# Performance work log

Measured on AMD Instinct MI355X. Metric: run time of the kernel, lower is better.

## Reference

```python
import jax, jax.numpy as jnp
import numpy as np

W = 5      # window size
H = 4      # num heads (num_channels)
EPS = 1e-6

def rmsnorm(x, w):
    return x * w * jax.lax.rsqrt(jnp.mean(x * x, axis=-1, keepdims=True) + EPS)

def dwconv3d(x, k):
    # x: [B,D0,D1,D2,C], k: [3,3,3,1,C] depthwise 3x3x3 conv, SAME padding
    return jax.lax.conv_general_dilated(
        x, k, (1, 1, 1), 'SAME',
        dimension_numbers=('NDHWC', 'DHWIO', 'NDHWC'),
        feature_group_count=x.shape[-1])

def _part(t):
    # [B,D0,D1,D2,C] -> [B*nw, W^3, C] non-overlapping 3D windows
    B, D0, D1, D2, C = t.shape
    t = t.reshape(B, D0 // W, W, D1 // W, W, D2 // W, W, C)
    t = t.transpose(0, 1, 3, 5, 2, 4, 6, 7)
    return t.reshape(-1, W ** 3, C)

def _unpart(t, B, D0, D1, D2):
    C = t.shape[-1]
    t = t.reshape(B, D0 // W, D1 // W, D2 // W, W, W, W, C)
    t = t.transpose(0, 1, 4, 2, 5, 3, 6, 7)
    return t.reshape(B, D0, D1, D2, C)

def _pool01(t):
    # mean-pool poolable_dims=(0,1) by factor W -> coarse grid
    B, D0, D1, D2, C = t.shape
    return t.reshape(B, D0 // W, W, D1 // W, W, D2, C).mean(axis=(2, 4))

def _mha(q, k, v):
    # q,k,v: [N, L, C] -> [N, L, C] multi-head attention
    N, L, C = q.shape
    dh = C // H
    q = q.reshape(N, L, H, dh)
    k = k.reshape(N, L, H, dh)
    v = v.reshape(N, L, H, dh)
    s = jnp.einsum('nqhd,nkhd->nhqk', q, k) * (1.0 / np.sqrt(dh))
    p = jax.nn.softmax(s, axis=-1)
    return jnp.einsum('nhqk,nkhd->nqhd', p, v).reshape(N, L, C)

def _hier_attn(x, qkv_w, qkv_b, proj_w, proj_b, dw_pre, dw_post, lr_down, lr_up):
    B, D0, D1, D2, C = x.shape
    # conv_position='both': pre depthwise-conv positional term
    xin = x + dwconv3d(x, dw_pre)
    qkv = xin @ qkv_w + qkv_b                     # [B,D0,D1,D2,3C]
    q, k, v = jnp.split(qkv, 3, axis=-1)
    # fine scale: windowed local attention in W^3 blocks
    fine = _unpart(_mha(_part(q), _part(k), _part(v)), B, D0, D1, D2)
    # coarse scale: pool dims (0,1) by W, global attention over coarse tokens
    qc, kc, vc = _pool01(q), _pool01(k), _pool01(v)
    Nc = qc.shape[1] * qc.shape[2] * qc.shape[3]
    oc = _mha(qc.reshape(B, Nc, C), kc.reshape(B, Nc, C), vc.reshape(B, Nc, C))
    oc = oc.reshape(B, D0 // W, D1 // W, D2, C)
    oc = jnp.repeat(jnp.repeat(oc, W, axis=1), W, axis=2)   # upsample to full grid
    # lowrank hierarchical merge of coarse branch into fine branch
    merged = fine + (oc @ lr_down) @ lr_up
    out = merged @ proj_w + proj_b
    out = out + xin                               # attn_residual
    out = out + dwconv3d(out, dw_post)            # post conv position
    return out

def setup_inputs() -> dict:
    key = jax.random.key(0)
    ks = jax.random.split(key, 8)
    B, D0, D1, D2, C = 4, 40, 40, 20, 256
    rank = C // 4
    s = 0.02
    return {
        'x': jax.random.normal(ks[0], (B, D0, D1, D2, C), jnp.float32),
        'norm1_w': jnp.ones((C,), jnp.float32),
        'attn_norm_w': jnp.ones((C,), jnp.float32),
        'qkv_w': jax.random.normal(ks[1], (C, 3 * C), jnp.float32) * s,
        'qkv_b': jnp.zeros((3 * C,), jnp.float32),
        'proj_w': jax.random.normal(ks[2], (C, C), jnp.float32) * s,
        'proj_b': jnp.zeros((C,), jnp.float32),
        'dw_pre': jax.random.normal(ks[3], (3, 3, 3, 1, C), jnp.float32) * s,
        'dw_post': jax.random.normal(ks[4], (3, 3, 3, 1, C), jnp.float32) * s,
        'lr_down': jax.random.normal(ks[5], (C, rank), jnp.float32) * s,
        'lr_up': jax.random.normal(ks[6], (rank, C), jnp.float32) * s,
    }

def reference(x, norm1_w, attn_norm_w, qkv_w, qkv_b, proj_w, proj_b,
              dw_pre, dw_post, lr_down, lr_up) -> jnp.ndarray:
    # x = x + attn_norm(hier_attn(norm1(x)))   (dropout inactive in eval)
    a = _hier_attn(rmsnorm(x, norm1_w), qkv_w, qkv_b, proj_w, proj_b,
                   dw_pre, dw_post, lr_down, lr_up)
    return x + rmsnorm(a, attn_norm_w)
```

## Files before the change

### kernel.cpp

```cpp
#include <hip/hip_runtime.h>

#define D0c 40
#define D1c 40
#define D2c 20
#define NVOX 128000

typedef __attribute__((ext_vector_type(4))) float f4;
typedef __attribute__((ext_vector_type(8))) __bf16 bf8;
typedef __attribute__((ext_vector_type(8))) unsigned short u8s;

static __device__ __forceinline__ unsigned short f2bf(float f) {
  union { float f; unsigned int u; } v; v.f = f;
  unsigned int r = v.u + 0x7fffu + ((v.u >> 16) & 1u);
  return (unsigned short)(r >> 16);
}
static __device__ __forceinline__ float bf2f(unsigned short h) {
  union { unsigned int u; float f; } v; v.u = ((unsigned int)h) << 16;
  return v.f;
}

#define MFMA16(a, b, c) __builtin_amdgcn_mfma_f32_16x16x32_bf16((a), (b), (c), 0, 0, 0)

static __device__ __forceinline__ void gload16(const void* g, void* l) {
  __builtin_amdgcn_global_load_lds((const __attribute__((address_space(1))) unsigned int*)g,
                                   (__attribute__((address_space(3))) unsigned int*)l, 16, 0, 0);
}

__global__ __launch_bounds__(256) void k_prepw(const float* __restrict__ qkv_w,
                                               const float* __restrict__ proj_w,
                                               unsigned short* __restrict__ wq,
                                               unsigned short* __restrict__ wp) {
  int id = blockIdx.x * 256 + threadIdx.x;
  if (id < 768 * 256) {
    int kk = id & 31, row = (id >> 5) & 127, kc = (id >> 12) & 7, nt = id >> 15;
    int s = kk >> 3, kj = kk & 7;
    int g = s ^ ((row >> 1) & 3);
    int k = kc * 32 + g * 8 + kj;
    int n = nt * 128 + row;
    wq[id] = f2bf(qkv_w[k * 768 + n]);
  } else {
    int j = id - 768 * 256;
    int kk = j & 31, row = (j >> 5) & 127, kc = (j >> 12) & 7, nt = j >> 15;
    int s = kk >> 3, kj = kk & 7;
    int g = s ^ ((row >> 1) & 3);
    int k = kc * 32 + g * 8 + kj;
    int n = nt * 128 + row;
    wp[j] = f2bf(proj_w[k * 256 + n]);
  }
}

__global__ __launch_bounds__(256) void k_rms1(const float* __restrict__ x,
                                              const float* __restrict__ w,
                                              unsigned short* __restrict__ xn) {
  int wv = threadIdx.x >> 6, ln = threadIdx.x & 63;
  int n = blockIdx.x * 4 + wv;
  f4 v = ((const f4*)(x + (size_t)n * 256))[ln];
  float ss = v.x * v.x + v.y * v.y + v.z * v.z + v.w * v.w;
#pragma unroll
  for (int m = 32; m >= 1; m >>= 1) ss += __shfl_xor(ss, m);
  float rs = rsqrtf(ss * (1.f / 256.f) + 1e-6f);
  f4 wv4 = ((const f4*)w)[ln];
  ushort4 o;
  o.x = f2bf(v.x * wv4.x * rs); o.y = f2bf(v.y * wv4.y * rs);
  o.z = f2bf(v.z * wv4.z * rs); o.w = f2bf(v.w * wv4.w * rs);
  ((ushort4*)(xn + (size_t)n * 256))[ln] = o;
}

__global__ __launch_bounds__(256) void k_convpre(const unsigned short* __restrict__ xn,
                                                 const float* __restrict__ dw,
                                                 unsigned short* __restrict__ xin) {
  int ch = threadIdx.x;
  int col = blockIdx.x;
  int z1 = col % D1c; int t = col / D1c; int z0 = t % D0c; int b = t / D0c;

  float W[27];
#pragma unroll
  for (int k = 0; k < 27; k++) W[k] = dw[k * 256 + ch];

  const unsigned short* base[9];
  bool val[9];
#pragma unroll
  for (int c = 0; c < 9; c++) {
    int dy = c / 3 - 1, dx = c % 3 - 1;
    int y0 = z0 + dy, y1 = z1 + dx;
    val[c] = ((unsigned)y0 < (unsigned)D0c) && ((unsigned)y1 < (unsigned)D1c);
    int yy0 = val[c] ? y0 : z0, yy1 = val[c] ? y1 : z1;
    base[c] = xn + ((size_t)((b * D0c + yy0) * D1c + yy1) * D2c) * 256 + ch;
  }
  float a0 = 0.f, a1 = 0.f, a2 = 0.f;
  unsigned short nxt[9];
#pragma unroll
  for (int c = 0; c < 9; c++) nxt[c] = val[c] ? base[c][0] : (unsigned short)0;
  unsigned short* op = xin + ((size_t)col * D2c) * 256 + ch;

  for (int z = 0; z < 20; z++) {
    float cf[9];
#pragma unroll
    for (int c = 0; c < 9; c++) cf[c] = bf2f(nxt[c]);
    int zn = (z < 19) ? (z + 1) : 19;
#pragma unroll
    for (int c = 0; c < 9; c++)
      nxt[c] = val[c] ? base[c][(size_t)zn * 256] : (unsigned short)0;
#pragma unroll
    for (int c = 0; c < 9; c++) {
      a0 += W[c * 3 + 2] * cf[c];
      a1 += W[c * 3 + 1] * cf[c];
      a2 += W[c * 3 + 0] * cf[c];
    }
    a1 += cf[4];
    if (z >= 1) {
      *op = f2bf(a0);
      op += 256;
    }
    a0 = a1; a1 = a2; a2 = 0.f;
  }
  *op = f2bf(a0);
}

__global__ __launch_bounds__(256) void k_gemm_qkv(const unsigned short* __restrict__ a_bf,
                                                  const unsigned short* __restrict__ wq2,
                                                  const float* __restrict__ bias,
                                                  unsigned short* __restrict__ out) {
  __shared__ unsigned short As[16384];
  __shared__ unsigned short Bs[8192];
  int m0 = blockIdx.x * 64;
  int tid = threadIdx.x;
  int w = tid >> 6, l = tid & 63;
  int wr = w >> 1, wc = w & 1;
  int lrow = l & 15, lg = l >> 4;

  {
    const char* Ab = (const char*)(a_bf + (size_t)m0 * 256);
    int row = tid >> 2, s = tid & 3;
    int g = s ^ ((row >> 1) & 3);
    const char* src0 = Ab + row * 512 + g * 16;
    char* dst0 = ((char*)As) + w * 1024 + l * 16;
#pragma unroll
    for (int kc = 0; kc < 8; kc++)
      gload16(src0 + kc * 64, dst0 + kc * 4096);
  }
  {
    const char* gB = (const char*)wq2;
    char* lB = (char*)Bs;
    gload16(gB + tid * 16, lB + w * 1024 + l * 16);
    gload16(gB + 4096 + tid * 16, lB + 4096 + w * 1024 + l * 16);
  }

  int buf = 0;
  f4 acc[2][4];
  for (int nt = 0; nt < 6; nt++) {
    float bvv[4];
#pragma unroll
    for (int j = 0; j < 4; j++) bvv[j] = bias[nt * 128 + wc * 64 + j * 16 + lrow];
#pragma unroll
    for (int i = 0; i < 2; i++)
#pragma unroll
      for (int j = 0; j < 4; j++) acc[i][j] = {0.f, 0.f, 0.f, 0.f};

    for (int kc = 0; kc < 8; kc++) {
      int t = nt * 8 + kc;
      if (t + 1 < 48) {
        const char* gB = (const char*)wq2 + (size_t)(t + 1) * 8192;
        char* lB = ((char*)Bs) + (buf ^ 1) * 8192;
        gload16(gB + tid * 16, lB + w * 1024 + l * 16);
        gload16(gB + 4096 + tid * 16, lB + 4096 + w * 1024 + l * 16);
        asm volatile("s_waitcnt vmcnt(2)\n\ts_barrier" ::: "memory");
      } else {
        asm volatile("s_waitcnt vmcnt(0)\n\ts_barrier" ::: "memory");
      }
      bf8 af[2], bf_[4];
#pragma unroll
      for (int i = 0; i < 2; i++) {
        int row = wr * 32 + i * 16 + lrow;
        af[i] = *(const bf8*)&As[kc * 2048 + row * 32 + ((lg ^ ((row >> 1) & 3)) * 8)];
      }
#pragma unroll
      for (int j = 0; j < 4; j++) {
        int rowb = wc * 64 + j * 16 + lrow;
        bf_[j] = *(const bf8*)&Bs[buf * 4096 + rowb * 32 + ((lg ^ ((rowb >> 1) & 3)) * 8)];
      }
#pragma unroll
      for (int i = 0; i < 2; i++)
#pragma unroll
        for (int j = 0; j < 4; j++) acc[i][j] = MFMA16(af[i], bf_[j], acc[i][j]);
      asm volatile("s_barrier" ::: "memory");
      buf ^= 1;
    }

    unsigned short* Cs = &Bs[(buf ^ 1) * 4096];
    int crow = tid >> 3, cseg = tid & 7;
#pragma unroll
    for (int h = 0; h < 2; h++) {
      if (wr == h) {
#pragma unroll
        for (int i = 0; i < 2; i++)
#pragma unroll
          for (int j = 0; j < 4; j++)
#pragma unroll
            for (int r = 0; r < 4; r++)
              Cs[(i * 16 + lg * 4 + r) * 128 + wc * 64 + j * 16 + lrow] =
                  f2bf(acc[i][j][r] + bvv[j]);
      }
      asm volatile("s_waitcnt lgkmcnt(0)\n\ts_barrier" ::: "memory");
      {
        u8s v0 = *(const u8s*)&Cs[crow * 128 + cseg * 16];
        u8s v1 = *(const u8s*)&Cs[crow * 128 + cseg * 16 + 8];
        unsigned short* orow = out + (size_t)(m0 + h * 32 + crow) * 768 + nt * 128 + cseg * 16;
        *(u8s*)orow = v0;
        *(u8s*)(orow + 8) = v1;
      }
      asm volatile("s_waitcnt lgkmcnt(0)\n\ts_barrier" ::: "memory");
    }
  }
}

__global__ __launch_bounds__(256) void k_fineattn(const unsigned short* __restrict__ qkv,
                                                  unsigned short* __restrict__ fine) {
  __shared__ unsigned short sm[27136];
  unsigned short* Qs = sm;
  unsigned short* Ks = sm + 9216;
  unsigned short* Vt = sm + 18432;
  unsigned short* Ps = sm;
  int h = blockIdx.x & 3, wid = blockIdx.x >> 2;
  int w2 = wid & 3, w1 = (wid >> 2) & 7, w0 = (wid >> 5) & 7, b = wid >> 8;
  int tid = threadIdx.x;
  int tok = tid >> 1, half = tid & 1;
  if (tok < 125) {
    int i0 = tok / 25, rr = tok % 25, i1 = rr / 5, i2 = rr % 5;
    int n = ((b * D0c + w0 * 5 + i0) * D1c + w1 * 5 + i1) * D2c + w2 * 5 + i2;
    const u8s* qp = (const u8s*)(qkv + (size_t)n * 768 + h * 64 + half * 32);
    const u8s* kp = (const u8s*)(qkv + (size_t)n * 768 + 256 + h * 64 + half * 32);
    const unsigned short* vp = qkv + (size_t)n * 768 + 512 + h * 64 + half * 32;
#pragma unroll
    for (int e = 0; e < 4; e++) {
      *(u8s*)&Qs[tok * 72 + half * 32 + e * 8] = qp[e];
      *(u8s*)&Ks[tok * 72 + half * 32 + e * 8] = kp[e];
    }
#pragma unroll
    for (int d = 0; d < 32; d++) Vt[(half * 32 + d) * 136 + tok] = vp[d];
  } else {
    u8s z = {0, 0, 0, 0, 0, 0, 0, 0};
#pragma unroll
    for (int e = 0; e < 4; e++) {
      *(u8s*)&Qs[tok * 72 + half * 32 + e * 8] = z;
      *(u8s*)&Ks[tok * 72 + half * 32 + e * 8] = z;
    }
#pragma unroll
    for (int d = 0; d < 32; d++) Vt[(half * 32 + d) * 136 + tok] = 0;
  }
  __syncthreads();
  int wv = tid >> 6, ln = tid & 63, lrow = ln & 15, lg = ln >> 4;
  f4 s[2][8];
#pragma unroll
  for (int mi = 0; mi < 2; mi++)
#pragma unroll
    for (int ni = 0; ni < 8; ni++) s[mi][ni] = {0.f, 0.f, 0.f, 0.f};
  bf8 aq[2][2];
#pragma unroll
  for (int ks = 0; ks < 2; ks++)
#pragma unroll
    for (int mi = 0; mi < 2; mi++)
      aq[mi][ks] = *(const bf8*)&Qs[(wv * 32 + mi * 16 + lrow) * 72 + ks * 32 + lg * 8];
#pragma unroll
  for (int ni = 0; ni < 8; ni++) {
#pragma unroll
    for (int ks = 0; ks < 2; ks++) {
      bf8 bk = *(const bf8*)&Ks[(ni * 16 + lrow) * 72 + ks * 32 + lg * 8];
      s[0][ni] = MFMA16(aq[0][ks], bk, s[0][ni]);
      s[1][ni] = MFMA16(aq[1][ks], bk, s[1][ni]);
    }
  }
#pragma unroll
  for (int mi = 0; mi < 2; mi++) {
#pragma unroll
    for (int j = 0; j < 4; j++) {
      float mx = -3e38f;
#pragma unroll
      for (int ni = 0; ni < 8; ni++) {
        int col = ni * 16 + lrow;
        float v = (col < 125) ? s[mi][ni][j] * 0.125f : -3e38f;
        s[mi][ni][j] = v;
        mx = fmaxf(mx, v);
      }
#pragma unroll
      for (int m = 8; m >= 1; m >>= 1) mx = fmaxf(mx, __shfl_xor(mx, m));
      float sum = 0.f;
#pragma unroll
      for (int ni = 0; ni < 8; ni++) {
        float p = __expf(s[mi][ni][j] - mx);
        s[mi][ni][j] = p;
        sum += p;
      }
#pragma unroll
      for (int m = 8; m >= 1; m >>= 1) sum += __shfl_xor(sum, m);
      float inv = 1.f / sum;
#pragma unroll
      for (int ni = 0; ni < 8; ni++) s[mi][ni][j] *= inv;
    }
  }
  __syncthreads();
#pragma unroll
  for (int mi = 0; mi < 2; mi++)
#pragma unroll
    for (int ni = 0; ni < 8; ni++)
#pragma unroll
      for (int j = 0; j < 4; j++)
        Ps[(wv * 32 + mi * 16 + lg * 4 + j) * 136 + ni * 16 + lrow] = f2bf(s[mi][ni][j]);
  __syncthreads();
  f4 o[2][4];
#pragma unroll
  for (int mi = 0; mi < 2; mi++)
#pragma unroll
    for (int ni = 0; ni < 4; ni++) o[mi][ni] = {0.f, 0.f, 0.f, 0.f};
#pragma unroll
  for (int ks = 0; ks < 4; ks++) {
    bf8 ap0 = *(const bf8*)&Ps[(wv * 32 + 0 + lrow) * 136 + ks * 32 + lg * 8];
    bf8 ap1 = *(const bf8*)&Ps[(wv * 32 + 16 + lrow) * 136 + ks * 32 + lg * 8];
#pragma unroll
    for (int ni = 0; ni < 4; ni++) {
      bf8 bv = *(const bf8*)&Vt[(ni * 16 + lrow) * 136 + ks * 32 + lg * 8];
      o[0][ni] = MFMA16(ap0, bv, o[0][ni]);
      o[1][ni] = MFMA16(ap1, bv, o[1][ni]);
    }
  }
#pragma unroll
  for (int mi = 0; mi < 2; mi++) {
    int rt0 = wv * 32 + mi * 16 + lg * 4;
#pragma unroll
    for (int r = 0; r < 4; r++) {
      int tk = rt0 + r;
      if (tk >= 125) continue;
      int i0 = tk / 25, rr = tk % 25, i1 = rr / 5, i2 = rr % 5;
      int n = ((b * D0c + w0 * 5 + i0) * D1c + w1 * 5 + i1) * D2c + w2 * 5 + i2;
#pragma unroll
      for (int ni = 0; ni < 4; ni++)
        fine[(size_t)n * 256 + h * 64 + ni * 16 + lrow] = f2bf(o[mi][ni][r]);
    }
  }
}

__global__ __launch_bounds__(128) void k_pool(const unsigned short* __restrict__ qkv,
                                              unsigned short* __restrict__ qc,
                                              unsigned short* __restrict__ kc,
                                              unsigned short* __restrict__ vct) {
  int ct = blockIdx.x;
  int tid = threadIdx.x;
  if (tid >= 96) return;
  int z2 = ct % 20; int t = ct / 20; int c1 = t & 7; int c0 = (t >> 3) & 7; int b = t >> 6;
  int off = tid * 8;
  f4 s0 = {0.f, 0.f, 0.f, 0.f}, s1 = {0.f, 0.f, 0.f, 0.f};
  for (int i0 = 0; i0 < 5; i0++)
    for (int i1 = 0; i1 < 5; i1++) {
      int n = ((b * D0c + c0 * 5 + i0) * D1c + c1 * 5 + i1) * D2c + z2;
      u8s v = *(const u8s*)(qkv + (size_t)n * 768 + off);
      s0.x += bf2f(v[0]); s0.y += bf2f(v[1]); s0.z += bf2f(v[2]); s0.w += bf2f(v[3]);
      s1.x += bf2f(v[4]); s1.y += bf2f(v[5]); s1.z += bf2f(v[6]); s1.w += bf2f(v[7]);
    }
  const float sc = 1.f / 25.f;
  s0.x *= sc; s0.y *= sc; s0.z *= sc; s0.w *= sc;
  s1.x *= sc; s1.y *= sc; s1.z *= sc; s1.w *= sc;
  if (off < 512) {
    unsigned short* dst = (off < 256) ? (qc + (size_t)ct * 256 + off)
                                      : (kc + (size_t)ct * 256 + (off - 256));
    u8s o;
    o[0] = f2bf(s0.x); o[1] = f2bf(s0.y); o[2] = f2bf(s0.z); o[3] = f2bf(s0.w);
    o[4] = f2bf(s1.x); o[5] = f2bf(s1.y); o[6] = f2bf(s1.z); o[7] = f2bf(s1.w);
    *(u8s*)dst = o;
  } else {
    int vch = off - 512;
    int h = vch >> 6, d0 = vch & 63;
    int tk = ct - b * 1280;
    unsigned short* vb = vct + (((size_t)b * 4 + h) * 64 + d0) * 1288 + tk;
    vb[0 * 1288] = f2bf(s0.x); vb[1 * 1288] = f2bf(s0.y);
    vb[2 * 1288] = f2bf(s0.z); vb[3 * 1288] = f2bf(s0.w);
    vb[4 * 1288] = f2bf(s1.x); vb[5 * 1288] = f2bf(s1.y);
    vb[6 * 1288] = f2bf(s1.z); vb[7 * 1288] = f2bf(s1.w);
  }
}

__global__ __launch_bounds__(256) void k_coarse(const unsigned short* __restrict__ qc,
                                                const unsigned short* __restrict__ kc,
                                                const unsigned short* __restrict__ vct,
                                                float* __restrict__ oc) {
  __shared__ unsigned short Qs[9216];
  __shared__ unsigned short KP[9216];
  __shared__ unsigned short Vts[4608];
  int qt = blockIdx.x;
  int b = blockIdx.y >> 2, h = blockIdx.y & 3;
  int tid = threadIdx.x, wv = tid >> 6, ln = tid & 63, lrow = ln & 15, lg = ln >> 4;
  {
    int tk = tid >> 1, half = tid & 1;
    const u8s* qp = (const u8s*)(qc + (size_t)(b * 1280 + qt * 128 + tk) * 256 + h * 64 + half * 32);
#pragma unroll
    for (int e = 0; e < 4; e++) *(u8s*)&Qs[tk * 72 + half * 32 + e * 8] = qp[e];
  }
  float mrun[2][4], srun[2][4];
  f4 o[2][4];
#pragma unroll
  for (int mi = 0; mi < 2; mi++)
#pragma unroll
    for (int j = 0; j < 4; j++) { mrun[mi][j] = -3e38f; srun[mi][j] = 0.f; }
#pragma unroll
  for (int mi = 0; mi < 2; mi++)
#pragma unroll
    for (int ni = 0; ni < 4; ni++) o[mi][ni] = {0.f, 0.f, 0.f, 0.f};

  int ktok = tid >> 2, kq = (tid & 3) * 16;
  int vd = tid >> 2, vtc = (tid & 3) * 16;

  for (int kt = 0; kt < 20; kt++) {
    {
      const u8s* kp = (const u8s*)(kc + (size_t)(b * 1280 + kt * 64 + ktok) * 256 + h * 64 + kq);
      *(u8s*)&KP[ktok * 72 + kq] = kp[0];
      *(u8s*)&KP[ktok * 72 + kq + 8] = kp[1];
      const u8s* vp = (const u8s*)(vct + (((size_t)b * 4 + h) * 64 + vd) * 1288 + kt * 64 + vtc);
      *(u8s*)&Vts[vd * 72 + vtc] = vp[0];
      *(u8s*)&Vts[vd * 72 + vtc + 8] = vp[1];
    }
    __syncthreads();
    f4 s[2][4];
#pragma unroll
    for (int mi = 0; mi < 2; mi++)
#pragma unroll
      for (int ni = 0; ni < 4; ni++) s[mi][ni] = {0.f, 0.f, 0.f, 0.f};
    bf8 aq[2][2];
#pragma unroll
    for (int ks = 0; ks < 2; ks++)
#pragma unroll
      for (int mi = 0; mi < 2; mi++)
        aq[mi][ks] = *(const bf8*)&Qs[(wv * 32 + mi * 16 + lrow) * 72 + ks * 32 + lg * 8];
#pragma unroll
    for (int ni = 0; ni < 4; ni++) {
#pragma unroll
      for (int ks = 0; ks < 2; ks++) {
        bf8 bk = *(const bf8*)&KP[(ni * 16 + lrow) * 72 + ks * 32 + lg * 8];
        s[0][ni] = MFMA16(aq[0][ks], bk, s[0][ni]);
        s[1][ni] = MFMA16(aq[1][ks], bk, s[1][ni]);
      }
    }
#pragma unroll
    for (int mi = 0; mi < 2; mi++) {
#pragma unroll
      for (int j = 0; j < 4; j++) {
        float mx = -3e38f;
#pragma unroll
        for (int ni = 0; ni < 4; ni++) {
          float v = s[mi][ni][j] * 0.125f;
          s[mi][ni][j] = v;
          mx = fmaxf(mx, v);
        }
#pragma unroll
        for (int m = 8; m >= 1; m >>= 1) mx = fmaxf(mx, __shfl_xor(mx, m));
        float nm = fmaxf(mrun[mi][j], mx);
        float alpha = __expf(mrun[mi][j] - nm);
        mrun[mi][j] = nm;
        float sum = 0.f;
#pragma unroll
        for (int ni = 0; ni < 4; ni++) {
          float p = __expf(s[mi][ni][j] - nm);
          s[mi][ni][j] = p;
          sum += p;
        }
#pragma unroll
        for (int m = 8; m >= 1; m >>= 1) sum += __shfl_xor(sum, m);
        srun[mi][j] = srun[mi][j] * alpha + sum;
#pragma unroll
        for (int ni = 0; ni < 4; ni++) o[mi][ni][j] *= alpha;
      }
    }
    __syncthreads();
#pragma unroll
    for (int mi = 0; mi < 2; mi++)
#pragma unroll
      for (int ni = 0; ni < 4; ni++)
#pragma unroll
        for (int j = 0; j < 4; j++)
          KP[(wv * 32 + mi * 16 + lg * 4 + j) * 72 + ni * 16 + lrow] = f2bf(s[mi][ni][j]);
    __syncthreads();
#pragma unroll
    for (int ks = 0; ks < 2; ks++) {
      bf8 ap0 = *(const bf8*)&KP[(wv * 32 + 0 + lrow) * 72 + ks * 32 + lg * 8];
      bf8 ap1 = *(const bf8*)&KP[(wv * 32 + 16 + lrow) * 72 + ks * 32 + lg * 8];
#pragma unroll
      for (int ni = 0; ni < 4; ni++) {
        bf8 bv = *(const bf8*)&Vts[(ni * 16 + lrow) * 72 + ks * 32 + lg * 8];
        o[0][ni] = MFMA16(ap0, bv, o[0][ni]);
        o[1][ni] = MFMA16(ap1, bv, o[1][ni]);
      }
    }
    __syncthreads();
  }
#pragma unroll
  for (int mi = 0; mi < 2; mi++)
#pragma unroll
    for (int j = 0; j < 4; j++) {
      float inv = 1.f / srun[mi][j];
      int row = qt * 128 + wv * 32 + mi * 16 + lg * 4 + j;
      float* orow = oc + ((size_t)(b * 1280 + row)) * 256 + h * 64;
#pragma unroll
      for (int ni = 0; ni < 4; ni++) orow[ni * 16 + lrow] = o[mi][ni][j] * inv;
    }
}

__global__ __launch_bounds__(256) void k_lowrank(const float* __restrict__ oc,
                                                 const float* __restrict__ lrd,
                                                 const float* __restrict__ lru,
                                                 float* __restrict__ oclr) {
  __shared__ float tmp[16 * 64];
  int t0 = blockIdx.x * 16;
  int tid = threadIdx.x;
  int i = tid >> 4, r4 = (tid & 15) * 4;
  f4 a = {0.f, 0.f, 0.f, 0.f};
  const float* orow = oc + (size_t)(t0 + i) * 256;
  for (int k = 0; k < 256; k++) {
    float ov = orow[k];
    const f4 w = *(const f4*)&lrd[k * 64 + r4];
    a.x += ov * w.x; a.y += ov * w.y; a.z += ov * w.z; a.w += ov * w.w;
  }
  *(f4*)&tmp[i * 64 + r4] = a;
  __syncthreads();
  int c16 = (tid & 15) * 16;
  f4 acc0 = {0.f,0.f,0.f,0.f}, acc1 = {0.f,0.f,0.f,0.f}, acc2 = {0.f,0.f,0.f,0.f}, acc3 = {0.f,0.f,0.f,0.f};
  for (int r = 0; r < 64; r++) {
    float tv = tmp[i * 64 + r];
    const f4* wr = (const f4*)&lru[r * 256 + c16];
    f4 w0 = wr[0], w1 = wr[1], w2 = wr[2], w3 = wr[3];
    acc0.x += tv * w0.x; acc0.y += tv * w0.y; acc0.z += tv * w0.z; acc0.w += tv * w0.w;
    acc1.x += tv * w1.x; acc1.y += tv * w1.y; acc1.z += tv * w1.z; acc1.w += tv * w1.w;
    acc2.x += tv * w2.x; acc2.y += tv * w2.y; acc2.z += tv * w2.z; acc2.w += tv * w2.w;
    acc3.x += tv * w3.x; acc3.y += tv * w3.y; acc3.z += tv * w3.z; acc3.w += tv * w3.w;
  }
  float* outr = oclr + (size_t)(t0 + i) * 256 + c16;
  *(f4*)&outr[0] = acc0; *(f4*)&outr[4] = acc1; *(f4*)&outr[8] = acc2; *(f4*)&outr[12] = acc3;
}

__global__ __launch_bounds__(256) void k_gemm_proj(const unsigned short* __restrict__ fine,
                                                   const float* __restrict__ oclr,
                                                   const unsigned short* __restrict__ wp2,
                                                   const float* __restrict__ bias,
                                                   const unsigned short* __restrict__ xin,
                                                   unsigned short* __restrict__ out1) {
  __shared__ unsigned short As[16384];
  __shared__ unsigned short Bs[8192];
  int m0 = blockIdx.x * 64;
  int tid = threadIdx.x;
  int w = tid >> 6, l = tid & 63;
  int wr = w >> 1, wc = w & 1;
  int lrow = l & 15, lg = l >> 4;

  {
    const char* gB = (const char*)wp2;
    char* lB = (char*)Bs;
    gload16(gB + tid * 16, lB + w * 1024 + l * 16);
    gload16(gB + 4096 + tid * 16, lB + 4096 + w * 1024 + l * 16);
  }
  {
    int row = tid >> 2, s = tid & 3;
    int g = s ^ ((row >> 1) & 3);
    int nrow = m0 + row;
    int z2 = nrow % D2c; int tt = nrow / D2c; int z1 = tt % D1c; tt /= D1c;
    int z0 = tt % D0c; int bb = tt / D0c;
    int ct = ((bb * 8 + z0 / 5) * 8 + z1 / 5) * 20 + z2;
    const unsigned short* fp = fine + (size_t)nrow * 256 + g * 8;
    const float* cp = oclr + (size_t)ct * 256 + g * 8;
#pragma unroll
    for (int kc = 0; kc < 8; kc++) {
      u8s fv = *(const u8s*)(fp + kc * 32);
      f4 cv0 = *(const f4*)(cp + kc * 32);
      f4 cv1 = *(const f4*)(cp + kc * 32 + 4);
      u8s t0;
      t0[0] = f2bf(bf2f(fv[0]) + cv0.x); t0[1] = f2bf(bf2f(fv[1]) + cv0.y);
      t0[2] = f2bf(bf2f(fv[2]) + cv0.z); t0[3] = f2bf(bf2f(fv[3]) + cv0.w);
      t0[4] = f2bf(bf2f(fv[4]) + cv1.x); t0[5] = f2bf(bf2f(fv[5]) + cv1.y);
      t0[6] = f2bf(bf2f(fv[6]) + cv1.z); t0[7] = f2bf(bf2f(fv[7]) + cv1.w);
      *(u8s*)&As[kc * 2048 + row * 32 + s * 8] = t0;
    }
  }
  asm volatile("s_waitcnt lgkmcnt(0)\n\ts_barrier" ::: "memory");

  int buf = 0;
  f4 acc[2][4];
  for (int nt = 0; nt < 2; nt++) {
    float bvv[4];
#pragma unroll
    for (int j = 0; j < 4; j++) bvv[j] = bias[nt * 128 + wc * 64 + j * 16 + lrow];
#pragma unroll
    for (int i = 0; i < 2; i++)
#pragma unroll
      for (int j = 0; j < 4; j++) acc[i][j] = {0.f, 0.f, 0.f, 0.f};

    for (int kc = 0; kc < 8; kc++) {
      int t = nt * 8 + kc;
      if (t + 1 < 16) {
        const char* gB = (const char*)wp2 + (size_t)(t + 1) * 8192;
        char* lB = ((char*)Bs) + (buf ^ 1) * 8192;
        gload16(gB + tid * 16, lB + w * 1024 + l * 16);
        gload16(gB + 4096 + tid * 16, lB + 4096 + w * 1024 + l * 16);
        asm volatile("s_waitcnt vmcnt(2)\n\ts_barrier" ::: "memory");
      } else {
        asm volatile("s_waitcnt vmcnt(0)\n\ts_barrier" ::: "memory");
      }
      bf8 af[2], bf_[4];
#pragma unroll
      for (int i = 0; i < 2; i++) {
        int row = wr * 32 + i * 16 + lrow;
        af[i] = *(const bf8*)&As[kc * 2048 + row * 32 + ((lg ^ ((row >> 1) & 3)) * 8)];
      }
#pragma unroll
      for (int j = 0; j < 4; j++) {
        int rowb = wc * 64 + j * 16 + lrow;
        bf_[j] = *(const bf8*)&Bs[buf * 4096 + rowb * 32 + ((lg ^ ((rowb >> 1) & 3)) * 8)];
      }
#pragma unroll
      for (int i = 0; i < 2; i++)
#pragma unroll
        for (int j = 0; j < 4; j++) acc[i][j] = MFMA16(af[i], bf_[j], acc[i][j]);
      asm volatile("s_barrier" ::: "memory");
      buf ^= 1;
    }

    unsigned short* Cs = &Bs[(buf ^ 1) * 4096];
    int crow = tid >> 3, cseg = tid & 7;
#pragma unroll
    for (int h = 0; h < 2; h++) {
      if (wr == h) {
#pragma unroll
        for (int i = 0; i < 2; i++)
#pragma unroll
          for (int j = 0; j < 4; j++)
#pragma unroll
            for (int r = 0; r < 4; r++)
              Cs[(i * 16 + lg * 4 + r) * 128 + wc * 64 + j * 16 + lrow] =
                  f2bf(acc[i][j][r] + bvv[j]);
      }
      asm volatile("s_waitcnt lgkmcnt(0)\n\ts_barrier" ::: "memory");
      {
        u8s v0 = *(const u8s*)&Cs[crow * 128 + cseg * 16];
        u8s v1 = *(const u8s*)&Cs[crow * 128 + cseg * 16 + 8];
        const unsigned short* xrow = xin + (size_t)(m0 + h * 32 + crow) * 256 + nt * 128 + cseg * 16;
        u8s x0 = *(const u8s*)xrow;
        u8s x1 = *(const u8s*)(xrow + 8);
        u8s o0, o1;
#pragma unroll
        for (int e = 0; e < 8; e++) {
          o0[e] = f2bf(bf2f(v0[e]) + bf2f(x0[e]));
          o1[e] = f2bf(bf2f(v1[e]) + bf2f(x1[e]));
        }
        unsigned short* orow = out1 + (size_t)(m0 + h * 32 + crow) * 256 + nt * 128 + cseg * 16;
        *(u8s*)orow = o0;
        *(u8s*)(orow + 8) = o1;
      }
      asm volatile("s_waitcnt lgkmcnt(0)\n\ts_barrier" ::: "memory");
    }
  }
}

__global__ __launch_bounds__(256) void k_convpost(const unsigned short* __restrict__ o1,
                                                  const float* __restrict__ dw,
                                                  const float* __restrict__ x,
                                                  const float* __restrict__ anw,
                                                  float* __restrict__ outp) {
  __shared__ float red[2][4];
  int ch = threadIdx.x, wv = ch >> 6, ln = ch & 63;
  int col = blockIdx.x;
  int z1 = col % D1c; int t = col / D1c; int z0 = t % D0c; int b = t / D0c;

  float W[27];
#pragma unroll
  for (int k = 0; k < 27; k++) W[k] = dw[k * 256 + ch];
  float wn = anw[ch];

  const unsigned short* base[9];
  bool val[9];
#pragma unroll
  for (int c = 0; c < 9; c++) {
    int dy = c / 3 - 1, dx = c % 3 - 1;
    int y0 = z0 + dy, y1 = z1 + dx;
    val[c] = ((unsigned)y0 < (unsigned)D0c) && ((unsigned)y1 < (unsigned)D1c);
    int yy0 = val[c] ? y0 : z0, yy1 = val[c] ? y1 : z1;
    base[c] = o1 + ((size_t)((b * D0c + yy0) * D1c + yy1) * D2c) * 256 + ch;
  }
  float a0 = 0.f, a1 = 0.f, a2 = 0.f;
  unsigned short nxt[9];
#pragma unroll
  for (int c = 0; c < 9; c++) nxt[c] = val[c] ? base[c][0] : (unsigned short)0;
  const float* xp = x + ((size_t)col * D2c) * 256 + ch;
  float* op = outp + ((size_t)col * D2c) * 256 + ch;

  for (int z = 0; z < 20; z++) {
    float cf[9];
#pragma unroll
    for (int c = 0; c < 9; c++) cf[c] = bf2f(nxt[c]);
    int zn = (z < 19) ? (z + 1) : 19;
#pragma unroll
    for (int c = 0; c < 9; c++)
      nxt[c] = val[c] ? base[c][(size_t)zn * 256] : (unsigned short)0;
#pragma unroll
    for (int c = 0; c < 9; c++) {
      a0 += W[c * 3 + 2] * cf[c];
      a1 += W[c * 3 + 1] * cf[c];
      a2 += W[c * 3 + 0] * cf[c];
    }
    a1 += cf[4];
    if (z >= 1) {
      float ss = a0 * a0;
#pragma unroll
      for (int m = 32; m >= 1; m >>= 1) ss += __shfl_xor(ss, m);
      int par = z & 1;
      if (ln == 0) red[par][wv] = ss;
      __syncthreads();
      float tot = red[par][0] + red[par][1] + red[par][2] + red[par][3];
      float rs = rsqrtf(tot * (1.f / 256.f) + 1e-6f);
      *op = *xp + a0 * wn * rs;
      op += 256; xp += 256;
    }
    a0 = a1; a1 = a2; a2 = 0.f;
  }
  {
    float ss = a0 * a0;
#pragma unroll
    for (int m = 32; m >= 1; m >>= 1) ss += __shfl_xor(ss, m);
    if (ln == 0) red[0][wv] = ss;
    __syncthreads();
    float tot = red[0][0] + red[0][1] + red[0][2] + red[0][3];
    float rs = rsqrtf(tot * (1.f / 256.f) + 1e-6f);
    *op = *xp + a0 * wn * rs;
  }
}

extern "C" void kernel_launch(void* const* d_in, const int* in_sizes, int n_in,
                              void* d_out, int out_size, void* d_ws, size_t ws_size,
                              hipStream_t stream) {
  const float* x          = (const float*)d_in[0];
  const float* norm1_w    = (const float*)d_in[1];
  const float* attn_norm_w= (const float*)d_in[2];
  const float* qkv_w      = (const float*)d_in[3];
  const float* qkv_b      = (const float*)d_in[4];
  const float* proj_w     = (const float*)d_in[5];
  const float* proj_b     = (const float*)d_in[6];
  const float* dw_pre     = (const float*)d_in[7];
  const float* dw_post    = (const float*)d_in[8];
  const float* lr_down    = (const float*)d_in[9];
  const float* lr_up      = (const float*)d_in[10];
  float* outp = (float*)d_out;

  unsigned char* w = (unsigned char*)d_ws;
  size_t off = 0;
  unsigned short* xn   = (unsigned short*)(w + off); off += 65536000ULL;
  unsigned short* xin  = (unsigned short*)(w + off); off += 65536000ULL;
  unsigned short* qkv  = (unsigned short*)(w + off); off += 196608000ULL;
  unsigned short* out1 = (unsigned short*)(w + off); off += 65536000ULL;
  unsigned short* qc   = (unsigned short*)(w + off); off += 2621440ULL;
  unsigned short* kc   = (unsigned short*)(w + off); off += 2621440ULL;
  unsigned short* vct  = (unsigned short*)(w + off); off += 2637824ULL;
  float* oc            = (float*)(w + off);          off += 5242880ULL;
  float* oclr          = (float*)(w + off);          off += 5242880ULL;
  unsigned short* wq   = (unsigned short*)(w + off); off += 393216ULL;
  unsigned short* wp   = (unsigned short*)(w + off); off += 131072ULL;
  unsigned short* fine = xn;

  k_prepw<<<1024, 256, 0, stream>>>(qkv_w, proj_w, wq, wp);
  k_rms1<<<32000, 256, 0, stream>>>(x, norm1_w, xn);
  k_convpre<<<6400, 256, 0, stream>>>(xn, dw_pre, xin);
  k_gemm_qkv<<<2000, 256, 0, stream>>>(xin, wq, qkv_b, qkv);
  k_fineattn<<<4096, 256, 0, stream>>>(qkv, fine);
  k_pool<<<5120, 128, 0, stream>>>(qkv, qc, kc, vct);
  k_coarse<<<dim3(10, 16), 256, 0, stream>>>(qc, kc, vct, oc);
  k_lowrank<<<320, 256, 0, stream>>>(oc, lr_down, lr_up, oclr);
  k_gemm_proj<<<2000, 256, 0, stream>>>(fine, oclr, wp, proj_b, xin, out1);
  k_convpost<<<6400, 256, 0, stream>>>(out1, dw_post, x, attn_norm_w, outp);
}
```

Baseline: 701.8 us.

## Vectorize depthwise convs: one wave per column, 4 channels per lane, zero-pad buffer

Both depthwise 3x3x3 conv kernels now map one wavefront to a spatial column, with each lane handling 4 channels through ushort4/f4 vector loads and stores. Previously each block handled a column with one channel per thread and scalar 2-byte loads. Out-of-bounds neighbours point at a shared zeroed pad buffer, so the per-load predicates are gone. Weights are staged in LDS, and loads are double-buffered two rows ahead. In convpost the RMS norm now reduces within a single wave, which removes the block barrier per output row. In exchange the kernels use more registers and about 27KB of LDS per block, and the grid shrinks by a factor of four.

```diff
diff --git a/kernel.cpp b/kernel.cpp
--- a/kernel.cpp
+++ b/kernel.cpp
@@ -26,10 +26,41 @@
                                    (__attribute__((address_space(3))) unsigned int*)l, 16, 0, 0);
 }
 
+#define CONV_LOAD(NB, R)                                                      \
+  do {                                                                        \
+    _Pragma("unroll") for (int c = 0; c < 9; c++)                             \
+        NB[c] = *(const ushort4*)(base[c] + (size_t)(R) * 256);               \
+  } while (0)
+
+#define CONV_CONSUME(NB)                                                      \
+  do {                                                                        \
+    f4 cf[9];                                                                 \
+    _Pragma("unroll") for (int c = 0; c < 9; c++) {                           \
+      cf[c].x = bf2f(NB[c].x); cf[c].y = bf2f(NB[c].y);                       \
+      cf[c].z = bf2f(NB[c].z); cf[c].w = bf2f(NB[c].w);                       \
+    }                                                                         \
+    _Pragma("unroll") for (int c = 0; c < 9; c++) {                           \
+      const f4 w0 = *(const f4*)&wl[(c * 3 + 0) * 256 + c0];                  \
+      const f4 w1 = *(const f4*)&wl[(c * 3 + 1) * 256 + c0];                  \
+      const f4 w2 = *(const f4*)&wl[(c * 3 + 2) * 256 + c0];                  \
+      a0 += w2 * cf[c]; a1 += w1 * cf[c]; a2 += w0 * cf[c];                   \
+    }                                                                         \
+    a1 += cf[4];                                                              \
+  } while (0)
+
+#define CONV_SHIFT()                                                          \
+  do { a0 = a1; a1 = a2; a2 = (f4){0.f, 0.f, 0.f, 0.f}; } while (0)
+
 __global__ __launch_bounds__(256) void k_prepw(const float* __restrict__ qkv_w,
                                                const float* __restrict__ proj_w,
                                                unsigned short* __restrict__ wq,
-                                               unsigned short* __restrict__ wp) {
+                                               unsigned short* __restrict__ wp,
+                                               unsigned short* __restrict__ zpad) {
+  if (blockIdx.x == 1024) {
+    u8s z = {0, 0, 0, 0, 0, 0, 0, 0};
+    for (int i = threadIdx.x; i < 768; i += 256) *(u8s*)(zpad + i * 8) = z;
+    return;
+  }
   int id = blockIdx.x * 256 + threadIdx.x;
   if (id < 768 * 256) {
     int kk = id & 31, row = (id >> 5) & 127, kc = (id >> 12) & 7, nt = id >> 15;
@@ -68,53 +99,69 @@
 
 __global__ __launch_bounds__(256) void k_convpre(const unsigned short* __restrict__ xn,
                                                  const float* __restrict__ dw,
+                                                 const unsigned short* __restrict__ zpad,
                                                  unsigned short* __restrict__ xin) {
-  int ch = threadIdx.x;
-  int col = blockIdx.x;
+  __shared__ float wl[6912];
+  for (int i = threadIdx.x; i < 6912; i += 256) wl[i] = dw[i];
+  __syncthreads();
+  int wv = threadIdx.x >> 6, ln = threadIdx.x & 63;
+  int col = blockIdx.x * 4 + wv;
   int z1 = col % D1c; int t = col / D1c; int z0 = t % D0c; int b = t / D0c;
-
-  float W[27];
-#pragma unroll
-  for (int k = 0; k < 27; k++) W[k] = dw[k * 256 + ch];
+  int c0 = ln * 4;
 
   const unsigned short* base[9];
-  bool val[9];
 #pragma unroll
   for (int c = 0; c < 9; c++) {
     int dy = c / 3 - 1, dx = c % 3 - 1;
     int y0 = z0 + dy, y1 = z1 + dx;
-    val[c] = ((unsigned)y0 < (unsigned)D0c) && ((unsigned)y1 < (unsigned)D1c);
-    int yy0 = val[c] ? y0 : z0, yy1 = val[c] ? y1 : z1;
-    base[c] = xn + ((size_t)((b * D0c + yy0) * D1c + yy1) * D2c) * 256 + ch;
-  }
-  float a0 = 0.f, a1 = 0.f, a2 = 0.f;
-  unsigned short nxt[9];
-#pragma unroll
-  for (int c = 0; c < 9; c++) nxt[c] = val[c] ? base[c][0] : (unsigned short)0;
-  unsigned short* op = xin + ((size_t)col * D2c) * 256 + ch;
-
-  for (int z = 0; z < 20; z++) {
-    float cf[9];
-#pragma unroll
-    for (int c = 0; c < 9; c++) cf[c] = bf2f(nxt[c]);
-    int zn = (z < 19) ? (z + 1) : 19;
-#pragma unroll
-    for (int c = 0; c < 9; c++)
-      nxt[c] = val[c] ? base[c][(size_t)zn * 256] : (unsigned short)0;
-#pragma unroll
-    for (int c = 0; c < 9; c++) {
-      a0 += W[c * 3 + 2] * cf[c];
-      a1 += W[c * 3 + 1] * cf[c];
-      a2 += W[c * 3 + 0] * cf[c];
-    }
-    a1 += cf[4];
-    if (z >= 1) {
-      *op = f2bf(a0);
-      op += 256;
-    }
-    a0 = a1; a1 = a2; a2 = 0.f;
-  }
-  *op = f2bf(a0);
+    bool valid = ((unsigned)y0 < (unsigned)D0c) && ((unsigned)y1 < (unsigned)D1c);
+    base[c] = valid ? (xn + ((size_t)((b * D0c + y0) * D1c + y1) * D2c) * 256 + c0)
+                    : (zpad + c0);
+  }
+  f4 a0 = {0.f,0.f,0.f,0.f}, a1 = {0.f,0.f,0.f,0.f}, a2 = {0.f,0.f,0.f,0.f};
+  ushort4 n0[9], n1[9];
+  CONV_LOAD(n0, 0);
+  CONV_LOAD(n1, 1);
+  unsigned short* op = xin + ((size_t)col * D2c) * 256 + c0;
+
+  CONV_CONSUME(n0);
+  CONV_SHIFT();
+  CONV_LOAD(n0, 2);
+  CONV_CONSUME(n1);
+  {
+    ushort4 o;
+    o.x = f2bf(a0.x); o.y = f2bf(a0.y); o.z = f2bf(a0.z); o.w = f2bf(a0.w);
+    *(ushort4*)op = o; op += 256;
+  }
+  CONV_SHIFT();
+  CONV_LOAD(n1, 3);
+
+  for (int z = 2; z < 20; z += 2) {
+    CONV_CONSUME(n0);
+    {
+      ushort4 o;
+      o.x = f2bf(a0.x); o.y = f2bf(a0.y); o.z = f2bf(a0.z); o.w = f2bf(a0.w);
+      *(ushort4*)op = o; op += 256;
+    }
+    CONV_SHIFT();
+    int r2 = (z + 2 > 19) ? 19 : (z + 2);
+    CONV_LOAD(n0, r2);
+
+    CONV_CONSUME(n1);
+    {
+      ushort4 o;
+      o.x = f2bf(a0.x); o.y = f2bf(a0.y); o.z = f2bf(a0.z); o.w = f2bf(a0.w);
+      *(ushort4*)op = o; op += 256;
+    }
+    CONV_SHIFT();
+    int r3 = (z + 3 > 19) ? 19 : (z + 3);
+    CONV_LOAD(n1, r3);
+  }
+  {
+    ushort4 o;
+    o.x = f2bf(a0.x); o.y = f2bf(a0.y); o.z = f2bf(a0.z); o.w = f2bf(a0.w);
+    *(ushort4*)op = o;
+  }
 }
 
 __global__ __launch_bounds__(256) void k_gemm_qkv(const unsigned short* __restrict__ a_bf,
@@ -657,75 +704,74 @@
 
 __global__ __launch_bounds__(256) void k_convpost(const unsigned short* __restrict__ o1,
                                                   const float* __restrict__ dw,
+                                                  const unsigned short* __restrict__ zpad,
                                                   const float* __restrict__ x,
                                                   const float* __restrict__ anw,
                                                   float* __restrict__ outp) {
-  __shared__ float red[2][4];
-  int ch = threadIdx.x, wv = ch >> 6, ln = ch & 63;
-  int col = blockIdx.x;
+  __shared__ float wl[6912];
+  for (int i = threadIdx.x; i < 6912; i += 256) wl[i] = dw[i];
+  __syncthreads();
+  int wv = threadIdx.x >> 6, ln = threadIdx.x & 63;
+  int col = blockIdx.x * 4 + wv;
   int z1 = col % D1c; int t = col / D1c; int z0 = t % D0c; int b = t / D0c;
-
-  float W[27];
-#pragma unroll
-  for (int k = 0; k < 27; k++) W[k] = dw[k * 256 + ch];
-  float wn = anw[ch];
+  int c0 = ln * 4;
 
   const unsigned short* base[9];
-  bool val[9];
 #pragma unroll
   for (int c = 0; c < 9; c++) {
     int dy = c / 3 - 1, dx = c % 3 - 1;
     int y0 = z0 + dy, y1 = z1 + dx;
-    val[c] = ((unsigned)y0 < (unsigned)D0c) && ((unsigned)y1 < (unsigned)D1c);
-    int yy0 = val[c] ? y0 : z0, yy1 = val[c] ? y1 : z1;
-    base[c] = o1 + ((size_t)((b * D0c + yy0) * D1c + yy1) * D2c) * 256 + ch;
-  }
-  float a0 = 0.f, a1 = 0.f, a2 = 0.f;
-  unsigned short nxt[9];
-#pragma unroll
-  for (int c = 0; c < 9; c++) nxt[c] = val[c] ? base[c][0] : (unsigned short)0;
-  const float* xp = x + ((size_t)col * D2c) * 256 + ch;
-  float* op = outp + ((size_t)col * D2c) * 256 + ch;
-
-  for (int z = 0; z < 20; z++) {
-    float cf[9];
-#pragma unroll
-    for (int c = 0; c < 9; c++) cf[c] = bf2f(nxt[c]);
-    int zn = (z < 19) ? (z + 1) : 19;
-#pragma unroll
-    for (int c = 0; c < 9; c++)
-      nxt[c] = val[c] ? base[c][(size_t)zn * 256] : (unsigned short)0;
-#pragma unroll
-    for (int c = 0; c < 9; c++) {
-      a0 += W[c * 3 + 2] * cf[c];
-      a1 += W[c * 3 + 1] * cf[c];
-      a2 += W[c * 3 + 0] * cf[c];
-    }
-    a1 += cf[4];
-    if (z >= 1) {
-      float ss = a0 * a0;
-#pragma unroll
-      for (int m = 32; m >= 1; m >>= 1) ss += __shfl_xor(ss, m);
-      int par = z & 1;
-      if (ln == 0) red[par][wv] = ss;
-      __syncthreads();
-      float tot = red[par][0] + red[par][1] + red[par][2] + red[par][3];
-      float rs = rsqrtf(tot * (1.f / 256.f) + 1e-6f);
-      *op = *xp + a0 * wn * rs;
-      op += 256; xp += 256;
-    }
-    a0 = a1; a1 = a2; a2 = 0.f;
-  }
-  {
-    float ss = a0 * a0;
-#pragma unroll
-    for (int m = 32; m >= 1; m >>= 1) ss += __shfl_xor(ss, m);
-    if (ln == 0) red[0][wv] = ss;
-    __syncthreads();
-    float tot = red[0][0] + red[0][1] + red[0][2] + red[0][3];
-    float rs = rsqrtf(tot * (1.f / 256.f) + 1e-6f);
-    *op = *xp + a0 * wn * rs;
-  }
+    bool valid = ((unsigned)y0 < (unsigned)D0c) && ((unsigned)y1 < (unsigned)D1c);
+    base[c] = valid ? (o1 + ((size_t)((b * D0c + y0) * D1c + y1) * D2c) * 256 + c0)
+                    : (zpad + c0);
+  }
+  f4 a0 = {0.f,0.f,0.f,0.f}, a1 = {0.f,0.f,0.f,0.f}, a2 = {0.f,0.f,0.f,0.f};
+  ushort4 n0[9], n1[9];
+  CONV_LOAD(n0, 0);
+  CONV_LOAD(n1, 1);
+  const f4 wv4 = *(const f4*)(anw + c0);
+  const float* xp = x + ((size_t)col * D2c) * 256 + c0;
+  float* op = outp + ((size_t)col * D2c) * 256 + c0;
+
+#define POST_STORE()                                                          \
+  do {                                                                        \
+    float ss = a0.x * a0.x + a0.y * a0.y + a0.z * a0.z + a0.w * a0.w;         \
+    _Pragma("unroll") for (int m = 32; m >= 1; m >>= 1)                       \
+        ss += __shfl_xor(ss, m);                                              \
+    float rs = rsqrtf(ss * (1.f / 256.f) + 1e-6f);                            \
+    f4 xv = *(const f4*)xp;                                                   \
+    f4 res;                                                                   \
+    res.x = xv.x + a0.x * wv4.x * rs;                                         \
+    res.y = xv.y + a0.y * wv4.y * rs;                                         \
+    res.z = xv.z + a0.z * wv4.z * rs;                                         \
+    res.w = xv.w + a0.w * wv4.w * rs;                                         \
+    *(f4*)op = res;                                                           \
+    xp += 256; op += 256;                                                     \
+  } while (0)
+
+  CONV_CONSUME(n0);
+  CONV_SHIFT();
+  CONV_LOAD(n0, 2);
+  CONV_CONSUME(n1);
+  POST_STORE();
+  CONV_SHIFT();
+  CONV_LOAD(n1, 3);
+
+  for (int z = 2; z < 20; z += 2) {
+    CONV_CONSUME(n0);
+    POST_STORE();
+    CONV_SHIFT();
+    int r2 = (z + 2 > 19) ? 19 : (z + 2);
+    CONV_LOAD(n0, r2);
+
+    CONV_CONSUME(n1);
+    POST_STORE();
+    CONV_SHIFT();
+    int r3 = (z + 3 > 19) ? 19 : (z + 3);
+    CONV_LOAD(n1, r3);
+  }
+  POST_STORE();
+#undef POST_STORE
 }
 
 extern "C" void kernel_launch(void* const* d_in, const int* in_sizes, int n_in,
@@ -757,16 +803,17 @@
   float* oclr          = (float*)(w + off);          off += 5242880ULL;
   unsigned short* wq   = (unsigned short*)(w + off); off += 393216ULL;
   unsigned short* wp   = (unsigned short*)(w + off); off += 131072ULL;
+  unsigned short* zpad = (unsigned short*)(w + off); off += 12288ULL;
   unsigned short* fine = xn;
 
-  k_prepw<<<1024, 256, 0, stream>>>(qkv_w, proj_w, wq, wp);
+  k_prepw<<<1025, 256, 0, stream>>>(qkv_w, proj_w, wq, wp, zpad);
   k_rms1<<<32000, 256, 0, stream>>>(x, norm1_w, xn);
-  k_convpre<<<6400, 256, 0, stream>>>(xn, dw_pre, xin);
+  k_convpre<<<1600, 256, 0, stream>>>(xn, dw_pre, zpad, xin);
   k_gemm_qkv<<<2000, 256, 0, stream>>>(xin, wq, qkv_b, qkv);
   k_fineattn<<<4096, 256, 0, stream>>>(qkv, fine);
   k_pool<<<5120, 128, 0, stream>>>(qkv, qc, kc, vct);
   k_coarse<<<dim3(10, 16), 256, 0, stream>>>(qc, kc, vct, oc);
   k_lowrank<<<320, 256, 0, stream>>>(oc, lr_down, lr_up, oclr);
   k_gemm_proj<<<2000, 256, 0, stream>>>(fine, oclr, wp, proj_b, xin, out1);
-  k_convpost<<<6400, 256, 0, stream>>>(out1, dw_post, x, attn_norm_w, outp);
-}
+  k_convpost<<<1600, 256, 0, stream>>>(out1, dw_post, zpad, x, attn_norm_w, outp);
+}
```

Result: faster. 617.3 us (-12.0%).
